# Kernel tuning notes

Hardware: AMD Instinct MI355X
Metric: run time of the kernel (lower is better)

The kernel has to match this reference:

```python
import jax, jax.numpy as jnp
import numpy as np
from jax import lax

B, N_BASES, C_IN, C_OUT, K, HW = 32, 5, 128, 128, 3, 56

def setup_inputs() -> dict:
    key = jax.random.key(0)
    k1, k2, k3 = jax.random.split(key, 3)
    x = jax.random.normal(k1, (B, C_IN, HW, HW), dtype=jnp.float32)
    weights = jax.random.normal(k2, (N_BASES, C_OUT, C_IN, K, K), dtype=jnp.float32) * 0.05
    scales = jax.random.uniform(k3, (N_BASES,), dtype=jnp.float32)
    return {"x": x, "weights": weights, "scales": scales}

def _binarize(w):
    # per-base: sign(w) * mean(|w|) over the whole weight tensor of that base
    m = jnp.mean(jnp.abs(w), axis=(1, 2, 3, 4), keepdims=True)  # [N,1,1,1,1]
    return jnp.sign(w) * m

def reference(x, weights, scales):
    # torch pads with constant value 1 (not zero) once, then all bases share it
    xp = jnp.pad(x, ((0, 0), (0, 0), (1, 1), (1, 1)), constant_values=1.0)
    wq = _binarize(weights)                              # [N,O,I,K,K]
    wf = wq.reshape(N_BASES * C_OUT, C_IN, K, K)          # fuse bases into one conv
    out = lax.conv_general_dilated(
        xp, wf, window_strides=(1, 1), padding='VALID',
        dimension_numbers=('NCHW', 'OIHW', 'NCHW'))      # [B, N*O, H, W]
    out = out.reshape(B, N_BASES, C_OUT, HW, HW)
    return jnp.einsum('bnohw,n->bohw', out, scales)
```

## Files before the change

kernel.cpp:

```cpp
#include <hip/hip_runtime.h>
#include <stdint.h>

#define N_BASES 5
#define WELEM (128 * 128 * 3 * 3)

typedef __attribute__((ext_vector_type(4))) float f32x4;
typedef __attribute__((ext_vector_type(8))) short bf16x8;

__device__ __forceinline__ unsigned short f2bf(float v) {
  union { float f; uint32_t u; } un;
  un.f = v;
  uint32_t r = un.u + 0x7FFFu + ((un.u >> 16) & 1u);
  return (unsigned short)(r >> 16);
}

__device__ __forceinline__ void glds16(const void* g, void* l) {
  __builtin_amdgcn_global_load_lds(
      (const __attribute__((address_space(1))) void*)g,
      (__attribute__((address_space(3))) void*)l, 16, 0, 0);
}

__global__ __launch_bounds__(256) void prep_fused(
    const float* __restrict__ x, const float* __restrict__ w,
    unsigned short* __restrict__ xp, float* __restrict__ csum_part) {
  int bi = blockIdx.x;
  if (bi >= 1856) {
    int id = bi - 1856;
    int n = id >> 6;
    int chunk = id & 63;
    const f32x4* wb = (const f32x4*)(w + (size_t)n * WELEM + chunk * 2304);
    float s = 0.f;
    for (int i = threadIdx.x; i < 576; i += 256) {
      f32x4 v = wb[i];
      s += fabsf(v.x) + fabsf(v.y) + fabsf(v.z) + fabsf(v.w);
    }
    #pragma unroll
    for (int off = 32; off > 0; off >>= 1) s += __shfl_down(s, off);
    __shared__ float red[4];
    if ((threadIdx.x & 63) == 0) red[threadIdx.x >> 6] = s;
    __syncthreads();
    if (threadIdx.x == 0) csum_part[id] = red[0] + red[1] + red[2] + red[3];
    return;
  }
  int b = bi / 58;
  int hp = bi - b * 58;
  unsigned short* dst = xp + ((size_t)b * 58 + hp) * 58 * 128;
  int gh = hp - 1;
  if ((unsigned)gh >= 56u) {
    uint4 ones = make_uint4(0x3F803F80u, 0x3F803F80u, 0x3F803F80u, 0x3F803F80u);
    for (int i = threadIdx.x; i < 928; i += 256) ((uint4*)dst)[i] = ones;
    return;
  }
  __shared__ unsigned short tile[128][61];
  const float* src = x + ((size_t)b * 128 * 56 + gh) * 56;
  for (int i = threadIdx.x; i < 128 * 14; i += 256) {
    int c = i / 14;
    int k = i - c * 14;
    f32x4 v = *(const f32x4*)(src + (size_t)c * 3136 + k * 4);
    tile[c][1 + 4 * k + 0] = f2bf(v.x);
    tile[c][1 + 4 * k + 1] = f2bf(v.y);
    tile[c][1 + 4 * k + 2] = f2bf(v.z);
    tile[c][1 + 4 * k + 3] = f2bf(v.w);
  }
  if (threadIdx.x < 128) {
    tile[threadIdx.x][0] = 0x3F80;
    tile[threadIdx.x][57] = 0x3F80;
  }
  __syncthreads();
  for (int i = threadIdx.x; i < 928; i += 256) {
    int wp = i >> 4;
    int c8 = i & 15;
    union { uint4 q; unsigned short h[8]; } u;
    #pragma unroll
    for (int j = 0; j < 8; ++j) u.h[j] = tile[c8 * 8 + j][wp];
    *(uint4*)(dst + (size_t)wp * 128 + c8 * 8) = u.q;
  }
}

__global__ __launch_bounds__(256) void binweight_kernel(
    const float* __restrict__ w, const float* __restrict__ csum_part,
    const float* __restrict__ scales, unsigned short* __restrict__ wq) {
  __shared__ float parts[320];
  __shared__ float coef[N_BASES];
  for (int i = threadIdx.x; i < 320; i += 256) parts[i] = csum_part[i];
  __syncthreads();
  if (threadIdx.x < N_BASES) {
    float s = 0.f;
    #pragma unroll 8
    for (int k = 0; k < 64; ++k) s += parts[threadIdx.x * 64 + k];
    coef[threadIdx.x] = scales[threadIdx.x] * s * (1.0f / (float)WELEM);
  }
  __syncthreads();
  int f = blockIdx.x * 256 + threadIdx.x;
  float s = 0.f;
  #pragma unroll
  for (int n = 0; n < N_BASES; ++n) {
    float cn = coef[n];
    float v = w[n * WELEM + f];
    s += (v > 0.f) ? cn : ((v < 0.f) ? -cn : 0.f);
  }
  int o = f / 1152;
  int rem = f - o * 1152;
  int i = rem / 9;
  int t = rem - i * 9;
  int half = i >> 6;
  int c8 = (i >> 3) & 7;
  int e = i & 7;
  wq[(size_t)(t * 2 + half) * 8192 + o * 64 + ((c8 ^ (o & 7)) << 3) + e] = f2bf(s);
}

__global__ __launch_bounds__(256, 2) void conv_kernel(
    const unsigned short* __restrict__ xp, const unsigned short* __restrict__ wq,
    float* __restrict__ out) {
  __shared__ unsigned short patch[23040];
  __shared__ unsigned short btile[2][8192];

  const int tid = threadIdx.x;
  const int blk = blockIdx.x;
  const int b = blk & 31;
  const int tile = blk >> 5;
  const int hi = tile >> 2;
  const int wi = tile & 3;
  const int h0 = hi * 8;
  const int w0 = (wi == 3) ? 40 : wi * 16;

  const int lane = tid & 63;
  const int wave = tid >> 6;

  {
    const unsigned short* g = wq + wave * 2048 + lane * 8;
    unsigned short* l = &btile[0][wave * 2048];
    #pragma unroll
    for (int j = 0; j < 4; ++j) glds16(g + j * 512, l + j * 512);
  }

  const size_t rowstride = 58 * 128;
  for (int i = tid; i < 2880; i += 256) {
    int sp = i >> 4;
    int c16 = i & 15;
    int ph = sp / 18;
    int pw = sp - ph * 18;
    const unsigned short* gp = xp + ((size_t)b * 58 + (h0 + ph)) * rowstride +
                               (size_t)(w0 + pw) * 128 + c16 * 8;
    uint4 v = *(const uint4*)gp;
    *(uint4*)&patch[sp * 128 + ((c16 ^ (sp & 7)) << 3)] = v;
  }
  __syncthreads();

  const int mh = wave >> 1;
  const int nh = wave & 1;
  const int l15 = lane & 15;
  const int quad = lane >> 4;

  f32x4 acc[4][4];
  #pragma unroll
  for (int mf = 0; mf < 4; ++mf)
    #pragma unroll
    for (int nf = 0; nf < 4; ++nf) acc[mf][nf] = (f32x4)0.f;

  #pragma unroll
  for (int t = 0; t < 9; ++t) {
    const int kh = t / 3;
    const int kw = t - kh * 3;
    int sp_mf[4];
    #pragma unroll
    for (int mf = 0; mf < 4; ++mf)
      sp_mf[mf] = (mh * 4 + mf + kh) * 18 + (l15 + kw);
    #pragma unroll
    for (int half = 0; half < 2; ++half) {
      const int s = t * 2 + half;
      if (s < 17) {
        const unsigned short* g =
            wq + (size_t)(s + 1) * 8192 + wave * 2048 + lane * 8;
        unsigned short* l = &btile[(s + 1) & 1][wave * 2048];
        #pragma unroll
        for (int j = 0; j < 4; ++j) glds16(g + j * 512, l + j * 512);
      }
      const unsigned short* bt = btile[s & 1];
      #pragma unroll
      for (int kk = 0; kk < 2; ++kk) {
        const int kb = half * 2 + kk;
        bf16x8 af[4], bfr[4];
        #pragma unroll
        for (int mf = 0; mf < 4; ++mf) {
          int sp = sp_mf[mf];
          af[mf] = *(const bf16x8*)&patch[sp * 128 +
                                          (((kb * 4 + quad) ^ (sp & 7)) << 3)];
        }
        #pragma unroll
        for (int nf = 0; nf < 4; ++nf) {
          int o = nh * 64 + nf * 16 + l15;
          bfr[nf] = *(const bf16x8*)&bt[o * 64 +
                                        (((kk * 4 + quad) ^ (o & 7)) << 3)];
        }
        #pragma unroll
        for (int mf = 0; mf < 4; ++mf)
          #pragma unroll
          for (int nf = 0; nf < 4; ++nf)
            acc[mf][nf] = __builtin_amdgcn_mfma_f32_16x16x32_bf16(
                af[mf], bfr[nf], acc[mf][nf], 0, 0, 0);
      }
      if (s < 17) {
        asm volatile("s_waitcnt vmcnt(0)" ::: "memory");
        asm volatile("s_barrier" ::: "memory");
      }
    }
  }

  #pragma unroll
  for (int mf = 0; mf < 4; ++mf) {
    int h = h0 + mh * 4 + mf;
    #pragma unroll
    for (int nf = 0; nf < 4; ++nf) {
      int o = nh * 64 + nf * 16 + l15;
      float* p = out + (((size_t)b * 128 + o) * 56 + h) * 56 + w0 + quad * 4;
      *(f32x4*)p = acc[mf][nf];
    }
  }
}

extern "C" void kernel_launch(void* const* d_in, const int* in_sizes, int n_in,
                              void* d_out, int out_size, void* d_ws, size_t ws_size,
                              hipStream_t stream) {
  const float* x = (const float*)d_in[0];
  const float* w = (const float*)d_in[1];
  const float* scales = (const float*)d_in[2];
  float* out = (float*)d_out;

  float* csum_part = (float*)d_ws;
  unsigned short* wq = (unsigned short*)((char*)d_ws + 4096);
  unsigned short* xpad = (unsigned short*)((char*)d_ws + 512 * 1024);

  prep_fused<<<1856 + 320, 256, 0, stream>>>(x, w, xpad, csum_part);
  binweight_kernel<<<576, 256, 0, stream>>>(w, csum_part, scales, wq);
  conv_kernel<<<56 * 16, 256, 0, stream>>>(xpad, wq, out);
}
```

Measured before the change: 148.3 us.

## Load conv weights directly from global into registers, drop LDS staging and barriers

The binarized weight tensor is relaid out so that each lane's 16-byte MFMA B-fragment is contiguous in global memory. The conv kernel now reads B fragments straight from global/L2 into registers instead of double-buffering them through LDS with per-step waitcnt and barrier. This frees 32KB of LDS per block, and the launch bound is raised to 3 blocks per SU to use that. The trade-off is global load latency on the MFMA critical path with no explicit prefetch, plus higher L2 traffic since every wave reloads the weights.

```diff
diff --git a/kernel.cpp b/kernel.cpp
--- a/kernel.cpp
+++ b/kernel.cpp
@@ -12,12 +12,6 @@
   un.f = v;
   uint32_t r = un.u + 0x7FFFu + ((un.u >> 16) & 1u);
   return (unsigned short)(r >> 16);
-}
-
-__device__ __forceinline__ void glds16(const void* g, void* l) {
-  __builtin_amdgcn_global_load_lds(
-      (const __attribute__((address_space(1))) void*)g,
-      (__attribute__((address_space(3))) void*)l, 16, 0, 0);
 }
 
 __global__ __launch_bounds__(256) void prep_fused(
@@ -103,17 +97,16 @@
   int rem = f - o * 1152;
   int i = rem / 9;
   int t = rem - i * 9;
-  int half = i >> 6;
-  int c8 = (i >> 3) & 7;
+  int kb = i >> 5;
+  int quad = (i >> 3) & 3;
   int e = i & 7;
-  wq[(size_t)(t * 2 + half) * 8192 + o * 64 + ((c8 ^ (o & 7)) << 3) + e] = f2bf(s);
-}
-
-__global__ __launch_bounds__(256, 2) void conv_kernel(
+  wq[((size_t)((t * 4 + kb) * 4 + quad) * 128 + o) * 8 + e] = f2bf(s);
+}
+
+__global__ __launch_bounds__(256, 3) void conv_kernel(
     const unsigned short* __restrict__ xp, const unsigned short* __restrict__ wq,
     float* __restrict__ out) {
   __shared__ unsigned short patch[23040];
-  __shared__ unsigned short btile[2][8192];
 
   const int tid = threadIdx.x;
   const int blk = blockIdx.x;
@@ -123,16 +116,6 @@
   const int wi = tile & 3;
   const int h0 = hi * 8;
   const int w0 = (wi == 3) ? 40 : wi * 16;
-
-  const int lane = tid & 63;
-  const int wave = tid >> 6;
-
-  {
-    const unsigned short* g = wq + wave * 2048 + lane * 8;
-    unsigned short* l = &btile[0][wave * 2048];
-    #pragma unroll
-    for (int j = 0; j < 4; ++j) glds16(g + j * 512, l + j * 512);
-  }
 
   const size_t rowstride = 58 * 128;
   for (int i = tid; i < 2880; i += 256) {
@@ -147,6 +130,8 @@
   }
   __syncthreads();
 
+  const int lane = tid & 63;
+  const int wave = tid >> 6;
   const int mh = wave >> 1;
   const int nh = wave & 1;
   const int l15 = lane & 15;
@@ -158,6 +143,9 @@
     #pragma unroll
     for (int nf = 0; nf < 4; ++nf) acc[mf][nf] = (f32x4)0.f;
 
+  const unsigned short* wlane =
+      wq + ((size_t)quad * 128 + nh * 64 + l15) * 8;
+
   #pragma unroll
   for (int t = 0; t < 9; ++t) {
     const int kh = t / 3;
@@ -167,43 +155,24 @@
     for (int mf = 0; mf < 4; ++mf)
       sp_mf[mf] = (mh * 4 + mf + kh) * 18 + (l15 + kw);
     #pragma unroll
-    for (int half = 0; half < 2; ++half) {
-      const int s = t * 2 + half;
-      if (s < 17) {
-        const unsigned short* g =
-            wq + (size_t)(s + 1) * 8192 + wave * 2048 + lane * 8;
-        unsigned short* l = &btile[(s + 1) & 1][wave * 2048];
+    for (int kb = 0; kb < 4; ++kb) {
+      bf16x8 af[4], bfr[4];
+      #pragma unroll
+      for (int nf = 0; nf < 4; ++nf)
+        bfr[nf] = *(const bf16x8*)(wlane + (size_t)(t * 4 + kb) * 4096 +
+                                   nf * 128);
+      #pragma unroll
+      for (int mf = 0; mf < 4; ++mf) {
+        int sp = sp_mf[mf];
+        af[mf] = *(const bf16x8*)&patch[sp * 128 +
+                                        (((kb * 4 + quad) ^ (sp & 7)) << 3)];
+      }
+      #pragma unroll
+      for (int mf = 0; mf < 4; ++mf)
         #pragma unroll
-        for (int j = 0; j < 4; ++j) glds16(g + j * 512, l + j * 512);
-      }
-      const unsigned short* bt = btile[s & 1];
-      #pragma unroll
-      for (int kk = 0; kk < 2; ++kk) {
-        const int kb = half * 2 + kk;
-        bf16x8 af[4], bfr[4];
-        #pragma unroll
-        for (int mf = 0; mf < 4; ++mf) {
-          int sp = sp_mf[mf];
-          af[mf] = *(const bf16x8*)&patch[sp * 128 +
-                                          (((kb * 4 + quad) ^ (sp & 7)) << 3)];
-        }
-        #pragma unroll
-        for (int nf = 0; nf < 4; ++nf) {
-          int o = nh * 64 + nf * 16 + l15;
-          bfr[nf] = *(const bf16x8*)&bt[o * 64 +
-                                        (((kk * 4 + quad) ^ (o & 7)) << 3)];
-        }
-        #pragma unroll
-        for (int mf = 0; mf < 4; ++mf)
-          #pragma unroll
-          for (int nf = 0; nf < 4; ++nf)
-            acc[mf][nf] = __builtin_amdgcn_mfma_f32_16x16x32_bf16(
-                af[mf], bfr[nf], acc[mf][nf], 0, 0, 0);
-      }
-      if (s < 17) {
-        asm volatile("s_waitcnt vmcnt(0)" ::: "memory");
-        asm volatile("s_barrier" ::: "memory");
-      }
+        for (int nf = 0; nf < 4; ++nf)
+          acc[mf][nf] = __builtin_amdgcn_mfma_f32_16x16x32_bf16(
+              af[mf], bfr[nf], acc[mf][nf], 0, 0, 0);
     }
   }
 
```

Result: slower. 180.5 us (+21.7%).
